# Optimization experiments

Hardware: AMD Instinct MI355X
Metric: run time of the kernel (lower is better)

## Reference

```python
import jax, jax.numpy as jnp
import numpy as np

EPS = 1e-9


def setup_inputs() -> dict:
    key = jax.random.key(0)
    kE, kQ, kK, kV = jax.random.split(key, 4)
    B, S, D = 8, 2048, 256
    return {
        "E": jax.random.normal(kE, (B, S, D), dtype=jnp.float32),
        "WQ": jax.random.normal(kQ, (D, D), dtype=jnp.float32) * (1.0 / np.sqrt(D)),
        "WK": jax.random.normal(kK, (D, D), dtype=jnp.float32) * (1.0 / np.sqrt(D)),
        "WV": jax.random.normal(kV, (D, D), dtype=jnp.float32) * (1.0 / np.sqrt(D)),
    }


def reference(E, WQ, WK, WV):
    # E: [B, S, D]; WQ/WK/WV: [D, D] (torch Linear weight, applied as x @ W.T)
    D = E.shape[-1]
    scale = jnp.asarray(np.sqrt(D), dtype=E.dtype)
    Q = jnp.einsum('bsd,ed->bse', E, WQ)
    K = jnp.einsum('bsd,ed->bse', E, WK)
    V = jnp.einsum('bsd,ed->bse', E, WV)
    # Full score matrix [B, S, S] (non-flash, as in the original)
    W = jnp.einsum('bqd,bkd->bqk', Q, K) / scale
    # mask=True path: causal tril mask, additionally zeroed where W == 0 exactly
    S_len = W.shape[-1]
    tril = jnp.tril(jnp.ones((S_len, S_len), dtype=W.dtype))  # [S, S]
    M = jnp.where(W == 0, jnp.zeros_like(W), tril[None, :, :])
    # custom masked softmax with epsilon denominator
    x_max = jnp.max(W, axis=-1, keepdims=True)
    x_exp = jnp.exp(W - x_max) * M
    A = x_exp / (jnp.sum(x_exp, axis=-1, keepdims=True) + EPS)
    return jnp.einsum('bqk,bkd->bqd', A, V)
```

## Files before the change

### kernel.cpp

```cpp
#include <hip/hip_runtime.h>
#include <stdint.h>


typedef __attribute__((ext_vector_type(8)))  short bf16x8;
typedef __attribute__((ext_vector_type(4)))  float f32x4;
typedef __attribute__((ext_vector_type(16))) float f32x16;

#define NEGF -3.0e38f
#define LDP  40

__device__ __forceinline__ unsigned short f2bf(float f){
  union { float f; unsigned u; } v; v.f = f;
  unsigned r = v.u + 0x7FFFu + ((v.u >> 16) & 1u);
  return (unsigned short)(r >> 16);
}
__device__ __forceinline__ unsigned pk2(float a, float b){
  return (unsigned)f2bf(a) | ((unsigned)f2bf(b) << 16);
}

__global__ void wconv_kernel(const float* __restrict__ WQ, const float* __restrict__ WK,
                             const float* __restrict__ WV, unsigned short* __restrict__ Wb)
{
  const int widx = blockIdx.x, kk = blockIdx.y, n = threadIdx.x;
  const float* W = (widx==0) ? WQ : ((widx==1) ? WK : WV);
  unsigned short* dst = Wb + (size_t)widx*65536 + kk*8192 + n*32;
#pragma unroll
  for (int gp=0; gp<4; ++gp){
    const int g = gp ^ (n & 3);
    const float* src = W + (size_t)n*256 + kk*32 + g*8;
    float4 a = *reinterpret_cast<const float4*>(src);
    float4 c = *reinterpret_cast<const float4*>(src + 4);
    uint4 v; v.x = pk2(a.x,a.y); v.y = pk2(a.z,a.w); v.z = pk2(c.x,c.y); v.w = pk2(c.z,c.w);
    *reinterpret_cast<uint4*>(dst + gp*8) = v;
  }
}

__global__ __launch_bounds__(256) void qkv_proj_kernel(
    const float* __restrict__ E, const unsigned short* __restrict__ Wb,
    unsigned short* __restrict__ Qb, unsigned short* __restrict__ Ka,
    unsigned short* __restrict__ Vf)
{
  __shared__ unsigned short As[32*256];
  __shared__ unsigned short Bs[2][8192];

  const int m0 = blockIdx.x * 32;
  const int b  = m0 >> 11;
  const int sb = m0 & 2047;
  const int t = threadIdx.x, lane = t & 63, w = t >> 6;
  const int hi = lane >> 4, lo = lane & 15;

  auto stageB = [&](int widx, int kk, int buf){
    const char* src = (const char*)Wb + widx*131072 + kk*16384;
    char* dst = (char*)Bs[buf];
#pragma unroll
    for (int c=0;c<4;c++){
      const int off = c*4096 + t*16;
      __builtin_amdgcn_global_load_lds(
        (const __attribute__((address_space(1))) unsigned int*)(src + off),
        (__attribute__((address_space(3))) unsigned int*)(dst + off), 16, 0, 0);
    }
  };

  stageB(0, 0, 0);
  {
    const int r = t >> 3, c0 = (t & 7) * 32;
    const float* ga = E + (size_t)(m0 + r)*256 + c0;
#pragma unroll
    for (int gg=0; gg<4; ++gg){
      float4 x = *reinterpret_cast<const float4*>(ga + gg*8);
      float4 y = *reinterpret_cast<const float4*>(ga + gg*8 + 4);
      uint4 v; v.x = pk2(x.x,x.y); v.y = pk2(x.z,x.w); v.z = pk2(y.x,y.y); v.w = pk2(y.z,y.w);
      const int g = (t & 7)*4 + gg;
      *reinterpret_cast<uint4*>((char*)As + r*512 + ((g ^ (r & 7)) << 4)) = v;
    }
  }
  __syncthreads();

  const f32x4 fzero = {0.f,0.f,0.f,0.f};
  const int u = sb >> 5;
  for (int widx=0; widx<3; ++widx){
    f32x4 acc[2][4];
#pragma unroll
    for (int mi=0;mi<2;mi++)
#pragma unroll
      for (int f=0;f<4;f++) acc[mi][f] = fzero;
    if (widx) stageB(widx, 0, 0);

    for (int kk=0; kk<8; ++kk){
      const int bb = kk & 1;
      asm volatile("s_waitcnt vmcnt(0)" ::: "memory");
      __syncthreads();
      if (kk < 7) stageB(widx, kk+1, bb^1);

      bf16x8 afr[2], bfr[4];
#pragma unroll
      for (int mi=0;mi<2;mi++){
        const int r = mi*16 + lo;
        afr[mi] = *reinterpret_cast<const bf16x8*>(
            (const char*)As + r*512 + (((kk*4 + hi) ^ (r & 7)) << 4));
      }
#pragma unroll
      for (int f=0;f<4;f++){
        const int n = w*64 + f*16 + lo;
        bfr[f] = *reinterpret_cast<const bf16x8*>(
            (const char*)Bs[bb] + n*64 + ((hi ^ (n & 3)) << 4));
      }
#pragma unroll
      for (int mi=0;mi<2;mi++)
#pragma unroll
        for (int f=0;f<4;f++)
          acc[mi][f] = __builtin_amdgcn_mfma_f32_16x16x32_bf16(afr[mi], bfr[f], acc[mi][f], 0,0,0);
    }

    if (widx == 0){
#pragma unroll
      for (int mi=0;mi<2;mi++)
#pragma unroll
        for (int f=0;f<4;f++){
          const int col = w*64 + f*16 + lo;
#pragma unroll
          for (int r=0;r<4;r++)
            Qb[(size_t)(m0 + mi*16 + hi*4 + r)*256 + col] = f2bf(acc[mi][f][r]*0.0625f);
        }
    } else if (widx == 1){
      unsigned short* Kab = Ka + (size_t)b*524288 + (size_t)u*8192;
#pragma unroll
      for (int mi=0;mi<2;mi++)
#pragma unroll
        for (int f=0;f<4;f++){
          const int c = w*4 + f;
          const int j = lo & 7;
          const int lb = 32*(lo>>3) + mi*16 + hi*4;
#pragma unroll
          for (int r=0;r<4;r++)
            Kab[(size_t)(c*64 + lb + r)*8 + j] = f2bf(acc[mi][f][r]);
        }
    } else {
      unsigned short* Vfb = Vf + (size_t)b*524288;
#pragma unroll
      for (int mi=0;mi<2;mi++)
#pragma unroll
        for (int f=0;f<4;f++){
          const int d  = w*64 + f*16 + lo;
          const int dt = d >> 5;
          const int l  = 32*(hi&1) + (d&31);
          const int j0 = 4*(hi>>1);
          unsigned short* vp = Vfb + ((size_t)((u*2 + mi)*8 + dt)*64 + l)*8 + j0;
          uint2 pw; pw.x = pk2(acc[mi][f][0], acc[mi][f][1]);
          pw.y = pk2(acc[mi][f][2], acc[mi][f][3]);
          *reinterpret_cast<uint2*>(vp) = pw;
        }
    }
  }
}

__global__ __launch_bounds__(256, 2) void attn_kernel(
    const unsigned short* __restrict__ Qb, const unsigned short* __restrict__ Ka,
    const unsigned short* __restrict__ Vf, float* __restrict__ Out,
    const int split, float* __restrict__ P1, float* __restrict__ ML)
{
  __shared__ char Kt[2][16384];

  const int bid  = blockIdx.x;
  const int b    = bid & 7;
  const int cidx = bid >> 3;
  int tau, chunk, mode, u0, u1;
  if (split){
    if (cidx < 32){
      tau = 31 - (cidx >> 1); chunk = cidx & 1;
      u0 = chunk ? (tau + 1) : 0;
      u1 = chunk ? (2*tau + 2) : (tau + 1);
      mode = 1 + chunk;
    } else { tau = 47 - cidx; chunk = 0; u0 = 0; u1 = 2*tau + 2; mode = 0; }
  } else { tau = 31 - cidx; chunk = 0; u0 = 0; u1 = 2*tau + 2; mode = 0; }
  const int Qbase = tau * 64;

  const int t = threadIdx.x;
  const int lane = t & 63, w = t >> 6;
  const int qs = w >> 1, dh = w & 1;
  const int l31 = lane & 31, h5 = lane >> 5;
  const int q_l = Qbase + qs*32 + l31;
  const int diagu = 2*tau + qs;

  const char* Kab = (const char*)Ka + (size_t)b*1048576;
  const char* Vfb = (const char*)Vf + (size_t)b*1048576;

  auto stage = [&](int uu){
    const char* src = Kab + (size_t)uu*16384;
    char* dstl = (char*)Kt[uu & 1];
#pragma unroll
    for (int i=0;i<4;i++){
      const int off = i*4096 + t*16;
      __builtin_amdgcn_global_load_lds(
        (const __attribute__((address_space(1))) unsigned int*)(src + off),
        (__attribute__((address_space(3))) unsigned int*)(dstl + off), 16, 0, 0);
    }
  };

  bf16x8 qf[16];
  {
    const unsigned short* Qp = Qb + ((size_t)(b*2048 + q_l))*256 + h5*8;
#pragma unroll
    for (int c=0;c<16;c++) qf[c] = *reinterpret_cast<const bf16x8*>(Qp + c*16);
  }

  const f32x16 z16 = {0.f,0.f,0.f,0.f,0.f,0.f,0.f,0.f,0.f,0.f,0.f,0.f,0.f,0.f,0.f,0.f};
  f32x16 accO[4];
#pragma unroll
  for (int i=0;i<4;i++) accO[i] = z16;
  float m_run = NEGF, l_run = 0.f;

  stage(u0);

  for (int u = u0; u < u1; ++u){
    asm volatile("s_waitcnt vmcnt(0)" ::: "memory");
    __builtin_amdgcn_s_barrier();
    if (u + 1 < u1) stage(u+1);

    const char* Vu = Vfb + (size_t)u*16384 + dh*4096 + lane*16;
    bf16x8 vf0[4], vf1[4];
#pragma unroll
    for (int i=0;i<4;i++){
      vf0[i] = *reinterpret_cast<const bf16x8*>(Vu + i*1024);
      vf1[i] = *reinterpret_cast<const bf16x8*>(Vu + 8192 + i*1024);
    }

    const char* kt = Kt[u & 1];
    f32x16 sv0 = z16, sv1 = z16;
#pragma unroll
    for (int c=0;c<16;c+=2){
      bf16x8 a0 = *reinterpret_cast<const bf16x8*>(kt + c*1024 + lane*16);
      bf16x8 a1 = *reinterpret_cast<const bf16x8*>(kt + (c+1)*1024 + lane*16);
      sv0 = __builtin_amdgcn_mfma_f32_32x32x16_bf16(a0, qf[c],   sv0, 0,0,0);
      sv1 = __builtin_amdgcn_mfma_f32_32x32x16_bf16(a1, qf[c+1], sv1, 0,0,0);
    }
    f32x16 s16 = sv0 + sv1;

    if (u >= diagu){
      const int kvb = u*32 + 4*h5;
#pragma unroll
      for (int r=0;r<16;r++){
        const int kv = kvb + (r&3) + 8*(r>>2);
        if (kv > q_l) s16[r] = NEGF;
      }
    }

    float t8[8], t4[4];
#pragma unroll
    for (int i=0;i<8;i++) t8[i] = fmaxf(s16[i], s16[i+8]);
#pragma unroll
    for (int i=0;i<4;i++) t4[i] = fmaxf(t8[i], t8[i+4]);
    float pmax = fmaxf(fmaxf(t4[0],t4[1]), fmaxf(t4[2],t4[3]));
    pmax = fmaxf(pmax, __shfl_xor(pmax, 32, 64));

    if (!__all(pmax - m_run <= 8.0f)){
      const float mn = fmaxf(m_run, pmax);
      const float alpha = __expf(m_run - mn);
#pragma unroll
      for (int i=0;i<4;i++) accO[i] *= alpha;
      l_run *= alpha;
      m_run = mn;
    }
    float p[16];
#pragma unroll
    for (int r=0;r<16;r++) p[r] = __expf(s16[r] - m_run);
#pragma unroll
    for (int i=0;i<8;i++) t8[i] = p[i] + p[i+8];
#pragma unroll
    for (int i=0;i<4;i++) t4[i] = t8[i] + t8[i+4];
    float ls = (t4[0]+t4[1]) + (t4[2]+t4[3]);
    ls += __shfl_xor(ls, 32, 64);
    l_run += ls;

    union { bf16x8 v; unsigned u32[4]; } pa0, pa1;
#pragma unroll
    for (int k=0;k<4;k++){
      pa0.u32[k] = pk2(p[2*k],   p[2*k+1]);
      pa1.u32[k] = pk2(p[8+2*k], p[9+2*k]);
    }

#pragma unroll
    for (int i=0;i<4;i++){
      accO[i] = __builtin_amdgcn_mfma_f32_32x32x16_bf16(vf0[i], pa0.v, accO[i], 0,0,0);
      accO[i] = __builtin_amdgcn_mfma_f32_32x32x16_bf16(vf1[i], pa1.v, accO[i], 0,0,0);
    }
  }

  if (mode && dh == 0 && lane < 32){
    float* mlp = ML + ((size_t)((b*16 + (tau-16))*2 + chunk)*64 + qs*32 + lane)*2;
    mlp[0] = m_run; mlp[1] = l_run;
  }

  __syncthreads();

  const float inv = (mode == 0) ? 1.0f/(l_run + 1e-9f) : 1.0f;
  float* Tw = (float*)(&Kt[0][0]) + w*2048;
  const int qloc = lane >> 1, dc = (lane & 1) * 16;
#pragma unroll
  for (int i=0;i<4;i++){
#pragma unroll
    for (int r=0;r<16;r++)
      Tw[l31*33 + ((r&3) + 8*(r>>2) + 4*h5)] = accO[i][r] * inv;
    asm volatile("s_waitcnt lgkmcnt(0)" ::: "memory");
    __builtin_amdgcn_sched_barrier(0);
    float* dst = (mode <= 1)
      ? (Out + ((size_t)(b*2048 + Qbase + qs*32 + qloc))*256 + dh*128 + i*32 + dc)
      : (P1 + ((size_t)((b*16 + (tau-16))*64 + qs*32 + qloc))*256 + dh*128 + i*32 + dc);
#pragma unroll
    for (int k=0;k<4;k++){
      float4 vv = { Tw[qloc*33 + dc + 4*k],     Tw[qloc*33 + dc + 4*k + 1],
                    Tw[qloc*33 + dc + 4*k + 2], Tw[qloc*33 + dc + 4*k + 3] };
      *reinterpret_cast<float4*>(dst + 4*k) = vv;
    }
    asm volatile("s_waitcnt lgkmcnt(0)" ::: "memory");
    __builtin_amdgcn_sched_barrier(0);
  }
}

__global__ void combine_kernel(float* __restrict__ Out, const float* __restrict__ P1,
                               const float* __restrict__ ML)
{
  const int bid = blockIdx.x;
  const int b = bid >> 4, tt = bid & 15;
  const int t = threadIdx.x;
  const int q = t >> 2, dg = (t & 3) * 64;
  const size_t mlb = ((size_t)(b*16 + tt)*2)*64 + q;
  const float m0 = ML[mlb*2],          l0 = ML[mlb*2 + 1];
  const float m1 = ML[(mlb + 64)*2],   l1 = ML[(mlb + 64)*2 + 1];
  const float M = fmaxf(m0, m1);
  const float e0 = __expf(m0 - M), e1 = __expf(m1 - M);
  const float inv = 1.0f/(e0*l0 + e1*l1 + 1e-9f);
  float* O = Out + ((size_t)(b*2048 + (16 + tt)*64 + q))*256 + dg;
  const float* P = P1 + ((size_t)((b*16 + tt)*64 + q))*256 + dg;
#pragma unroll
  for (int k=0;k<16;k++){
    float4 a = *reinterpret_cast<const float4*>(O + k*4);
    float4 c = *reinterpret_cast<const float4*>(P + k*4);
    float4 o;
    o.x = (e0*a.x + e1*c.x)*inv; o.y = (e0*a.y + e1*c.y)*inv;
    o.z = (e0*a.z + e1*c.z)*inv; o.w = (e0*a.w + e1*c.w)*inv;
    *reinterpret_cast<float4*>(O + k*4) = o;
  }
}

extern "C" void kernel_launch(void* const* d_in, const int* in_sizes, int n_in,
                              void* d_out, int out_size, void* d_ws, size_t ws_size,
                              hipStream_t stream)
{
  const float* E  = (const float*)d_in[0];
  const float* WQ = (const float*)d_in[1];
  const float* WK = (const float*)d_in[2];
  const float* WV = (const float*)d_in[3];
  const size_t elems = (size_t)8*2048*256;

  unsigned short* Qb = (unsigned short*)d_ws;
  unsigned short* Ka = Qb + elems;
  unsigned short* Vf = Ka + elems;
  unsigned short* Wb = Vf + elems;
  float* P1 = (float*)((char*)d_ws + 3*elems*2 + 393216);
  float* ML = P1 + (size_t)8*16*64*256;

  const size_t NEED_MIN  = 3*elems*2 + 393216;
  const size_t NEED_FULL = NEED_MIN + ((size_t)8*16*64*256 + 32768)*4;
  if (ws_size < NEED_MIN) return;
  const int split = (ws_size >= NEED_FULL) ? 1 : 0;

  wconv_kernel<<<dim3(3,8), 256, 0, stream>>>(WQ, WK, WV, Wb);
  qkv_proj_kernel<<<512, 256, 0, stream>>>(E, Wb, Qb, Ka, Vf);
  attn_kernel<<<split ? 384 : 256, 256, 0, stream>>>(Qb, Ka, Vf, (float*)d_out, split, P1, ML);
  if (split) combine_kernel<<<128, 256, 0, stream>>>((float*)d_out, P1, ML);
}
```

Measured before the change: 101.3 us.

## Split all query tiles in two, stage V through LDS, triple-pipeline loads

The attention kernel now splits every query tile into two key-range chunks instead of only the 16 longest, giving 512 blocks. It double-buffers both K and V tiles through LDS with one-tile lookahead instead of loading V straight from global memory. The second-chunk partials are stored as bf16 to halve their traffic, and the combine kernel merges all tiles. The QKV projection gets a different wait/barrier pipeline and an occupancy hint. The risks are extra combine work for short tiles, more LDS per block that may limit occupancy, and bf16 rounding of partial outputs.

```diff
diff --git a/kernel.cpp b/kernel.cpp
--- a/kernel.cpp
+++ b/kernel.cpp
@@ -6,8 +6,8 @@
 typedef __attribute__((ext_vector_type(4)))  float f32x4;
 typedef __attribute__((ext_vector_type(16))) float f32x16;
 
-#define NEGF -3.0e38f
-#define LDP  40
+#define NEGF  -3.0e38f
+#define MINIT -1.0e30f
 
 __device__ __forceinline__ unsigned short f2bf(float f){
   union { float f; unsigned u; } v; v.f = f;
@@ -16,6 +16,9 @@
 }
 __device__ __forceinline__ unsigned pk2(float a, float b){
   return (unsigned)f2bf(a) | ((unsigned)f2bf(b) << 16);
+}
+__device__ __forceinline__ float bf2f(unsigned short h){
+  union { unsigned u; float f; } v; v.u = ((unsigned)h) << 16; return v.f;
 }
 
 __global__ void wconv_kernel(const float* __restrict__ WQ, const float* __restrict__ WK,
@@ -35,7 +38,7 @@
   }
 }
 
-__global__ __launch_bounds__(256) void qkv_proj_kernel(
+__global__ __launch_bounds__(256, 3) void qkv_proj_kernel(
     const float* __restrict__ E, const unsigned short* __restrict__ Wb,
     unsigned short* __restrict__ Qb, unsigned short* __restrict__ Ka,
     unsigned short* __restrict__ Vf)
@@ -74,7 +77,6 @@
       *reinterpret_cast<uint4*>((char*)As + r*512 + ((g ^ (r & 7)) << 4)) = v;
     }
   }
-  __syncthreads();
 
   const f32x4 fzero = {0.f,0.f,0.f,0.f};
   const int u = sb >> 5;
@@ -88,9 +90,12 @@
 
     for (int kk=0; kk<8; ++kk){
       const int bb = kk & 1;
-      asm volatile("s_waitcnt vmcnt(0)" ::: "memory");
-      __syncthreads();
       if (kk < 7) stageB(widx, kk+1, bb^1);
+      if (kk < 7) asm volatile("s_waitcnt vmcnt(4) lgkmcnt(0)" ::: "memory");
+      else        asm volatile("s_waitcnt vmcnt(0) lgkmcnt(0)" ::: "memory");
+      __builtin_amdgcn_sched_barrier(0);
+      __builtin_amdgcn_s_barrier();
+      __builtin_amdgcn_sched_barrier(0);
 
       bf16x8 afr[2], bfr[4];
 #pragma unroll
@@ -110,6 +115,10 @@
 #pragma unroll
         for (int f=0;f<4;f++)
           acc[mi][f] = __builtin_amdgcn_mfma_f32_16x16x32_bf16(afr[mi], bfr[f], acc[mi][f], 0,0,0);
+
+      asm volatile("s_waitcnt lgkmcnt(0)" ::: "memory");
+      __builtin_amdgcn_sched_barrier(0);
+      __builtin_amdgcn_s_barrier();
     }
 
     if (widx == 0){
@@ -157,22 +166,22 @@
 __global__ __launch_bounds__(256, 2) void attn_kernel(
     const unsigned short* __restrict__ Qb, const unsigned short* __restrict__ Ka,
     const unsigned short* __restrict__ Vf, float* __restrict__ Out,
-    const int split, float* __restrict__ P1, float* __restrict__ ML)
+    const int sched, unsigned short* __restrict__ Pb, float* __restrict__ ML)
 {
-  __shared__ char Kt[2][16384];
+  __shared__ char Lds[2][32768];
 
   const int bid  = blockIdx.x;
   const int b    = bid & 7;
-  const int cidx = bid >> 3;
+  const int slot = bid >> 3;
   int tau, chunk, mode, u0, u1;
-  if (split){
-    if (cidx < 32){
-      tau = 31 - (cidx >> 1); chunk = cidx & 1;
-      u0 = chunk ? (tau + 1) : 0;
-      u1 = chunk ? (2*tau + 2) : (tau + 1);
-      mode = 1 + chunk;
-    } else { tau = 47 - cidx; chunk = 0; u0 = 0; u1 = 2*tau + 2; mode = 0; }
-  } else { tau = 31 - cidx; chunk = 0; u0 = 0; u1 = 2*tau + 2; mode = 0; }
+  if (sched){
+    tau = 31 - (slot >> 1); chunk = slot & 1;
+    u0 = chunk ? (tau + 1) : 0;
+    u1 = chunk ? (2*tau + 2) : (tau + 1);
+    mode = 1 + chunk;
+  } else {
+    tau = 31 - slot; chunk = 0; u0 = 0; u1 = 2*tau + 2; mode = 0;
+  }
   const int Qbase = tau * 64;
 
   const int t = threadIdx.x;
@@ -185,15 +194,20 @@
   const char* Kab = (const char*)Ka + (size_t)b*1048576;
   const char* Vfb = (const char*)Vf + (size_t)b*1048576;
 
-  auto stage = [&](int uu){
-    const char* src = Kab + (size_t)uu*16384;
-    char* dstl = (char*)Kt[uu & 1];
+  auto stage = [&](int uu, int buf){
+    const char* gk = Kab + (size_t)uu*16384;
+    const char* gv = Vfb + (size_t)uu*16384;
+    char* lk = Lds[buf];
+    char* lv = Lds[buf] + 16384;
 #pragma unroll
     for (int i=0;i<4;i++){
       const int off = i*4096 + t*16;
       __builtin_amdgcn_global_load_lds(
-        (const __attribute__((address_space(1))) unsigned int*)(src + off),
-        (__attribute__((address_space(3))) unsigned int*)(dstl + off), 16, 0, 0);
+        (const __attribute__((address_space(1))) unsigned int*)(gk + off),
+        (__attribute__((address_space(3))) unsigned int*)(lk + off), 16, 0, 0);
+      __builtin_amdgcn_global_load_lds(
+        (const __attribute__((address_space(1))) unsigned int*)(gv + off),
+        (__attribute__((address_space(3))) unsigned int*)(lv + off), 16, 0, 0);
     }
   };
 
@@ -208,24 +222,22 @@
   f32x16 accO[4];
 #pragma unroll
   for (int i=0;i<4;i++) accO[i] = z16;
-  float m_run = NEGF, l_run = 0.f;
-
-  stage(u0);
+  float m_run = MINIT, l_run = 0.f;
+
+  stage(u0, 0);
+  if (u0 + 1 < u1) stage(u0 + 1, 1);
 
   for (int u = u0; u < u1; ++u){
-    asm volatile("s_waitcnt vmcnt(0)" ::: "memory");
+    const int buf = (u - u0) & 1;
+    if (u + 1 < u1) asm volatile("s_waitcnt vmcnt(8)" ::: "memory");
+    else            asm volatile("s_waitcnt vmcnt(0)" ::: "memory");
+    __builtin_amdgcn_sched_barrier(0);
     __builtin_amdgcn_s_barrier();
-    if (u + 1 < u1) stage(u+1);
-
-    const char* Vu = Vfb + (size_t)u*16384 + dh*4096 + lane*16;
-    bf16x8 vf0[4], vf1[4];
-#pragma unroll
-    for (int i=0;i<4;i++){
-      vf0[i] = *reinterpret_cast<const bf16x8*>(Vu + i*1024);
-      vf1[i] = *reinterpret_cast<const bf16x8*>(Vu + 8192 + i*1024);
-    }
-
-    const char* kt = Kt[u & 1];
+    __builtin_amdgcn_sched_barrier(0);
+
+    const char* kt = Lds[buf];
+    const char* lv = Lds[buf] + 16384 + dh*4096 + lane*16;
+
     f32x16 sv0 = z16, sv1 = z16;
 #pragma unroll
     for (int c=0;c<16;c+=2){
@@ -236,6 +248,13 @@
     }
     f32x16 s16 = sv0 + sv1;
 
+    bf16x8 vf0[4], vf1[4];
+#pragma unroll
+    for (int i=0;i<4;i++){
+      vf0[i] = *reinterpret_cast<const bf16x8*>(lv + i*1024);
+      vf1[i] = *reinterpret_cast<const bf16x8*>(lv + 8192 + i*1024);
+    }
+
     if (u >= diagu){
       const int kvb = u*32 + 4*h5;
 #pragma unroll
@@ -284,17 +303,20 @@
       accO[i] = __builtin_amdgcn_mfma_f32_32x32x16_bf16(vf0[i], pa0.v, accO[i], 0,0,0);
       accO[i] = __builtin_amdgcn_mfma_f32_32x32x16_bf16(vf1[i], pa1.v, accO[i], 0,0,0);
     }
+
+    asm volatile("s_waitcnt lgkmcnt(0)" ::: "memory");
+    __builtin_amdgcn_sched_barrier(0);
+    __builtin_amdgcn_s_barrier();
+    if (u + 2 < u1) stage(u + 2, buf);
   }
 
   if (mode && dh == 0 && lane < 32){
-    float* mlp = ML + ((size_t)((b*16 + (tau-16))*2 + chunk)*64 + qs*32 + lane)*2;
+    float* mlp = ML + ((size_t)(((b*32 + tau)*2 + chunk)*64 + qs*32 + lane))*2;
     mlp[0] = m_run; mlp[1] = l_run;
   }
 
-  __syncthreads();
-
   const float inv = (mode == 0) ? 1.0f/(l_run + 1e-9f) : 1.0f;
-  float* Tw = (float*)(&Kt[0][0]) + w*2048;
+  float* Tw = (float*)(&Lds[0][0]) + w*2048;
   const int qloc = lane >> 1, dc = (lane & 1) * 16;
 #pragma unroll
   for (int i=0;i<4;i++){
@@ -303,43 +325,57 @@
       Tw[l31*33 + ((r&3) + 8*(r>>2) + 4*h5)] = accO[i][r] * inv;
     asm volatile("s_waitcnt lgkmcnt(0)" ::: "memory");
     __builtin_amdgcn_sched_barrier(0);
-    float* dst = (mode <= 1)
-      ? (Out + ((size_t)(b*2048 + Qbase + qs*32 + qloc))*256 + dh*128 + i*32 + dc)
-      : (P1 + ((size_t)((b*16 + (tau-16))*64 + qs*32 + qloc))*256 + dh*128 + i*32 + dc);
-#pragma unroll
-    for (int k=0;k<4;k++){
-      float4 vv = { Tw[qloc*33 + dc + 4*k],     Tw[qloc*33 + dc + 4*k + 1],
-                    Tw[qloc*33 + dc + 4*k + 2], Tw[qloc*33 + dc + 4*k + 3] };
-      *reinterpret_cast<float4*>(dst + 4*k) = vv;
+    const float* srcT = &Tw[qloc*33 + dc];
+    if (mode < 2){
+      float* dst = Out + ((size_t)(b*2048 + Qbase + qs*32 + qloc))*256 + dh*128 + i*32 + dc;
+#pragma unroll
+      for (int k=0;k<4;k++){
+        float4 vv = { srcT[4*k], srcT[4*k+1], srcT[4*k+2], srcT[4*k+3] };
+        *reinterpret_cast<float4*>(dst + 4*k) = vv;
+      }
+    } else {
+      unsigned short* pb = Pb + (((size_t)(b*32 + tau)*64 + qs*32 + qloc))*256
+                              + dh*128 + i*32 + dc;
+      uint4 w0, w1;
+      w0.x = pk2(srcT[0],  srcT[1]);  w0.y = pk2(srcT[2],  srcT[3]);
+      w0.z = pk2(srcT[4],  srcT[5]);  w0.w = pk2(srcT[6],  srcT[7]);
+      w1.x = pk2(srcT[8],  srcT[9]);  w1.y = pk2(srcT[10], srcT[11]);
+      w1.z = pk2(srcT[12], srcT[13]); w1.w = pk2(srcT[14], srcT[15]);
+      *reinterpret_cast<uint4*>(pb)     = w0;
+      *reinterpret_cast<uint4*>(pb + 8) = w1;
     }
     asm volatile("s_waitcnt lgkmcnt(0)" ::: "memory");
     __builtin_amdgcn_sched_barrier(0);
   }
 }
 
-__global__ void combine_kernel(float* __restrict__ Out, const float* __restrict__ P1,
+__global__ void combine_kernel(float* __restrict__ Out, const unsigned short* __restrict__ Pb,
                                const float* __restrict__ ML)
 {
-  const int bid = blockIdx.x;
-  const int b = bid >> 4, tt = bid & 15;
+  const int b = blockIdx.x & 7, tt = blockIdx.x >> 3;
   const int t = threadIdx.x;
   const int q = t >> 2, dg = (t & 3) * 64;
-  const size_t mlb = ((size_t)(b*16 + tt)*2)*64 + q;
-  const float m0 = ML[mlb*2],          l0 = ML[mlb*2 + 1];
-  const float m1 = ML[(mlb + 64)*2],   l1 = ML[(mlb + 64)*2 + 1];
-  const float M = fmaxf(m0, m1);
+  const float* mlp = ML + ((size_t)((b*32 + tt)*2)*64)*2;
+  const float m0 = mlp[q*2],            l0 = mlp[q*2 + 1];
+  const float m1 = mlp[(64 + q)*2],     l1 = mlp[(64 + q)*2 + 1];
+  const float M  = fmaxf(m0, m1);
   const float e0 = __expf(m0 - M), e1 = __expf(m1 - M);
   const float inv = 1.0f/(e0*l0 + e1*l1 + 1e-9f);
-  float* O = Out + ((size_t)(b*2048 + (16 + tt)*64 + q))*256 + dg;
-  const float* P = P1 + ((size_t)((b*16 + tt)*64 + q))*256 + dg;
-#pragma unroll
-  for (int k=0;k<16;k++){
-    float4 a = *reinterpret_cast<const float4*>(O + k*4);
-    float4 c = *reinterpret_cast<const float4*>(P + k*4);
-    float4 o;
-    o.x = (e0*a.x + e1*c.x)*inv; o.y = (e0*a.y + e1*c.y)*inv;
-    o.z = (e0*a.z + e1*c.z)*inv; o.w = (e0*a.w + e1*c.w)*inv;
-    *reinterpret_cast<float4*>(O + k*4) = o;
+  float* O = Out + ((size_t)(b*2048 + tt*64 + q))*256 + dg;
+  const unsigned short* P = Pb + ((size_t)((b*32 + tt)*64 + q))*256 + dg;
+#pragma unroll
+  for (int k=0;k<8;k++){
+    float4 a0 = *reinterpret_cast<const float4*>(O + 8*k);
+    float4 a1 = *reinterpret_cast<const float4*>(O + 8*k + 4);
+    uint4 pv = *reinterpret_cast<const uint4*>(P + 8*k);
+    const unsigned short* us = (const unsigned short*)&pv;
+    float4 o0, o1;
+    o0.x = (e0*a0.x + e1*bf2f(us[0]))*inv; o0.y = (e0*a0.y + e1*bf2f(us[1]))*inv;
+    o0.z = (e0*a0.z + e1*bf2f(us[2]))*inv; o0.w = (e0*a0.w + e1*bf2f(us[3]))*inv;
+    o1.x = (e0*a1.x + e1*bf2f(us[4]))*inv; o1.y = (e0*a1.y + e1*bf2f(us[5]))*inv;
+    o1.z = (e0*a1.z + e1*bf2f(us[6]))*inv; o1.w = (e0*a1.w + e1*bf2f(us[7]))*inv;
+    *reinterpret_cast<float4*>(O + 8*k)     = o0;
+    *reinterpret_cast<float4*>(O + 8*k + 4) = o1;
   }
 }
 
@@ -357,16 +393,17 @@
   unsigned short* Ka = Qb + elems;
   unsigned short* Vf = Ka + elems;
   unsigned short* Wb = Vf + elems;
-  float* P1 = (float*)((char*)d_ws + 3*elems*2 + 393216);
-  float* ML = P1 + (size_t)8*16*64*256;
-
-  const size_t NEED_MIN  = 3*elems*2 + 393216;
-  const size_t NEED_FULL = NEED_MIN + ((size_t)8*16*64*256 + 32768)*4;
-  if (ws_size < NEED_MIN) return;
-  const int split = (ws_size >= NEED_FULL) ? 1 : 0;
+  const size_t base = 3*elems*2 + 393216;
+
+  const size_t PB = (size_t)8*32*64*256*2;
+  const size_t MLSZ = (size_t)8*32*2*64*2*4;
+  if (ws_size < base) return;
+  const int sched = (ws_size >= base + PB + MLSZ) ? 1 : 0;
+  unsigned short* Pb = (unsigned short*)((char*)d_ws + base);
+  float* ML = (float*)((char*)d_ws + base + PB);
 
   wconv_kernel<<<dim3(3,8), 256, 0, stream>>>(WQ, WK, WV, Wb);
   qkv_proj_kernel<<<512, 256, 0, stream>>>(E, Wb, Qb, Ka, Vf);
-  attn_kernel<<<split ? 384 : 256, 256, 0, stream>>>(Qb, Ka, Vf, (float*)d_out, split, P1, ML);
-  if (split) combine_kernel<<<128, 256, 0, stream>>>((float*)d_out, P1, ML);
-}
+  attn_kernel<<<sched ? 512 : 256, 256, 0, stream>>>(Qb, Ka, Vf, (float*)d_out, sched, Pb, ML);
+  if (sched) combine_kernel<<<256, 256, 0, stream>>>((float*)d_out, Pb, ML);
+}
```

Result: faster. 89.19 us (-11.9%).
